# Kernel optimization log

Hardware: AMD Instinct MI355X
Metric: run time of the kernel (lower is better)

## Reference

```python
import jax, jax.numpy as jnp
import numpy as np

B, N, H = 2, 8192, 128
EPS = 1e-06


def setup_inputs() -> dict:
    key = jax.random.key(0)
    k1, k2, k3, k4 = jax.random.split(key, 4)
    x = jax.random.normal(k1, (B, N, H), dtype=jnp.float32)
    # adjacency is sparse in the original (tf.sparse); represented dense here
    # for the reference math (same result as sparse_dense_matmul).
    adj = jax.random.normal(k2, (B, N, N), dtype=jnp.float32)
    W = jax.random.normal(k3, (H, H), dtype=jnp.float32)
    b = jax.random.normal(k4, (H,), dtype=jnp.float32)
    return {"x": x, "adj": adj, "W": W, "b": b}


def reference(x, adj, W, b):
    # in-degree over |adj|, per batch, per node: [B, N]
    in_degrees = jnp.sum(jnp.abs(adj), axis=-1)
    # symmetric-ish degree normalization: [B, N, 1]
    norm = jnp.power(in_degrees + EPS, -0.5)[..., None]
    # dense projection: [B, N, H]
    support = jnp.matmul(x, W)
    # batched SpMM (dense equivalent) with pre/post degree norm
    out = jnp.einsum("bmn,bnh->bmh", adj, support * norm) * norm
    return jax.nn.elu(out + b)
```

## Files before the change

### kernel.cpp

```cpp
#include <hip/hip_runtime.h>
#include <hip/hip_bf16.h>
#include <math.h>

#define NN 8192
#define HD 128
#define NB 2
#define EPSF 1e-6f
#define BM 32
#define BK 128
#define NSTEP (NN / BK)

typedef __attribute__((ext_vector_type(8))) __bf16 bf16x8;
typedef __attribute__((ext_vector_type(4))) float f32x4;

__global__ __launch_bounds__(256) void k_degree(const float* __restrict__ adj,
                                                float* __restrict__ norm) {
    const int row  = blockIdx.x * 4 + (threadIdx.x >> 6);
    const int lane = threadIdx.x & 63;
    const float4* p = (const float4*)(adj + (size_t)row * NN);
    float s = 0.f;
#pragma unroll
    for (int i = 0; i < 32; ++i) {
        float4 v = p[(size_t)i * 64 + lane];
        s += fabsf(v.x) + fabsf(v.y) + fabsf(v.z) + fabsf(v.w);
    }
#pragma unroll
    for (int off = 32; off > 0; off >>= 1) s += __shfl_down(s, off);
    if (lane == 0) norm[row] = rsqrtf(s + EPSF);
}

__global__ __launch_bounds__(256) void k_support(const float* __restrict__ x,
                                                 const float* __restrict__ W,
                                                 const float* __restrict__ norm,
                                                 __hip_bfloat16* __restrict__ snT) {
    const int b  = blockIdx.x >> 9;
    const int n0 = (blockIdx.x & 511) * 16;
    __shared__ float xs[16][132];
    const int t = threadIdx.x;
    {
        const int r = t >> 4, c0 = (t & 15) * 8;
        const float* src = x + ((size_t)(b * NN + n0 + r)) * HD + c0;
        *(float4*)&xs[r][c0]     = *(const float4*)src;
        *(float4*)&xs[r][c0 + 4] = *(const float4*)(src + 4);
    }
    __syncthreads();
    const int nl = t & 15;
    const int h0 = (t >> 4) * 8;
    float s[8] = {0.f,0.f,0.f,0.f,0.f,0.f,0.f,0.f};
#pragma unroll 4
    for (int k = 0; k < HD; ++k) {
        const float xv = xs[nl][k];
        const float* wr = W + k * HD + h0;
        float4 wa = *(const float4*)wr;
        float4 wb = *(const float4*)(wr + 4);
        s[0] += xv * wa.x; s[1] += xv * wa.y; s[2] += xv * wa.z; s[3] += xv * wa.w;
        s[4] += xv * wb.x; s[5] += xv * wb.y; s[6] += xv * wb.z; s[7] += xv * wb.w;
    }
    const float nv = norm[b * NN + n0 + nl];
#pragma unroll
    for (int hb = 0; hb < 8; ++hb)
        snT[((size_t)b * HD + h0 + hb) * NN + n0 + nl] = __float2bfloat16(s[hb] * nv);
}

__device__ __forceinline__ bf16x8 cvt8(float4 a, float4 b) {
    bf16x8 r;
    r[0] = (__bf16)a.x; r[1] = (__bf16)a.y; r[2] = (__bf16)a.z; r[3] = (__bf16)a.w;
    r[4] = (__bf16)b.x; r[5] = (__bf16)b.y; r[6] = (__bf16)b.z; r[7] = (__bf16)b.w;
    return r;
}

__device__ __forceinline__ void gload_lds16(const float* g, void* l) {
    __builtin_amdgcn_global_load_lds(
        (const __attribute__((address_space(1))) void*)g,
        (__attribute__((address_space(3))) void*)l, 16, 0, 0);
}

__global__ __launch_bounds__(256, 4) void k_gemm8(const float* __restrict__ adj,
                                                  const __hip_bfloat16* __restrict__ snT,
                                                  const float* __restrict__ norm,
                                                  const float* __restrict__ bias,
                                                  float* __restrict__ out) {
    const int b    = blockIdx.y;
    const int swz  = (blockIdx.x & 7) * 32 + (blockIdx.x >> 3);
    const int m0   = swz * BM;
    const int w    = threadIdx.x >> 6;
    const int lane = threadIdx.x & 63;
    const int fr   = lane & 15;
    const int g    = lane >> 4;

    const float* adjB = adj + (size_t)b * NN * NN;
    const __hip_bfloat16* snB = snT + (size_t)b * HD * NN;

    __shared__ __align__(16) char Abuf[2][BM * BK * 4];

    const float* sptr[4];
#pragma unroll
    for (int c = 0; c < 4; ++c) {
        const int fg   = (w * 4 + c) * 64 + lane;
        const int row  = fg >> 5;
        const int gsrc = (fg & 31) ^ (row & 7);
        sptr[c] = adjB + (size_t)(m0 + row) * NN + gsrc * 4;
    }

    const __hip_bfloat16* bp0 = snB + (size_t)(w * 32 + fr) * NN + g * 8;
    const __hip_bfloat16* bp1 = bp0 + (size_t)16 * NN;

    f32x4 acc[2][2] = {};
    const int xr = fr & 7;

#pragma unroll
    for (int c = 0; c < 4; ++c)
        gload_lds16(sptr[c], &Abuf[0][(w * 4 + c) * 1024]);

#pragma unroll 1
    for (int s = 0; s < NSTEP; ++s) {
        __syncthreads();
        const char* lb = Abuf[s & 1];

        bf16x8 Bf[2][4];
#pragma unroll
        for (int ks = 0; ks < 4; ++ks) {
            Bf[0][ks] = *(const bf16x8*)(bp0 + s * BK + ks * 32);
            Bf[1][ks] = *(const bf16x8*)(bp1 + s * BK + ks * 32);
        }

        if (s + 1 < NSTEP) {
            char* nb = Abuf[(s + 1) & 1];
#pragma unroll
            for (int c = 0; c < 4; ++c)
                gload_lds16(sptr[c] + (s + 1) * BK, &nb[(w * 4 + c) * 1024]);
        }

#pragma unroll
        for (int mt = 0; mt < 2; ++mt) {
            const char* rbase = lb + (mt * 16 + fr) * 512;
#pragma unroll
            for (int ks = 0; ks < 4; ++ks) {
                float4 fa = *(const float4*)(rbase + ((ks * 8 + ((g * 2 + 0) ^ xr)) << 4));
                float4 fb = *(const float4*)(rbase + ((ks * 8 + ((g * 2 + 1) ^ xr)) << 4));
                bf16x8 af = cvt8(fa, fb);
                acc[mt][0] = __builtin_amdgcn_mfma_f32_16x16x32_bf16(af, Bf[0][ks], acc[mt][0], 0, 0, 0);
                acc[mt][1] = __builtin_amdgcn_mfma_f32_16x16x32_bf16(af, Bf[1][ks], acc[mt][1], 0, 0, 0);
            }
        }
    }

    const float* normB = norm + b * NN + m0;
    float* outB = out + ((size_t)b * NN + m0) * HD;
#pragma unroll
    for (int mt = 0; mt < 2; ++mt)
#pragma unroll
        for (int ht = 0; ht < 2; ++ht) {
            const int h  = w * 32 + ht * 16 + fr;
            const float bv = bias[h];
#pragma unroll
            for (int j = 0; j < 4; ++j) {
                const int r = mt * 16 + g * 4 + j;
                float v = acc[mt][ht][j] * normB[r] + bv;
                v = v > 0.f ? v : expm1f(v);
                outB[(size_t)r * HD + h] = v;
            }
        }
}

extern "C" void kernel_launch(void* const* d_in, const int* in_sizes, int n_in,
                              void* d_out, int out_size, void* d_ws, size_t ws_size,
                              hipStream_t stream) {
    (void)in_sizes; (void)n_in; (void)out_size; (void)ws_size;
    const float* x    = (const float*)d_in[0];
    const float* adj  = (const float*)d_in[1];
    const float* W    = (const float*)d_in[2];
    const float* bias = (const float*)d_in[3];
    float* out = (float*)d_out;

    float* norm = (float*)d_ws;
    __hip_bfloat16* snT = (__hip_bfloat16*)((char*)d_ws + 65536);

    k_degree <<<dim3(NB * NN / 4),  dim3(256), 0, stream>>>(adj, norm);
    k_support<<<dim3(NB * NN / 16), dim3(256), 0, stream>>>(x, W, norm, snT);
    k_gemm8  <<<dim3(NN / BM, NB),  dim3(256), 0, stream>>>(adj, snT, norm, bias, out);
}
```

Before: 280.2 us.

## Deepen adjacency prefetch to four LDS stages with register double-buffered B fragments

```diff
diff --git a/kernel.cpp b/kernel.cpp
--- a/kernel.cpp
+++ b/kernel.cpp
@@ -75,7 +75,7 @@
         (__attribute__((address_space(3))) void*)l, 16, 0, 0);
 }
 
-__global__ __launch_bounds__(256, 4) void k_gemm8(const float* __restrict__ adj,
+__global__ __launch_bounds__(256, 2) void k_gemm9(const float* __restrict__ adj,
                                                   const __hip_bfloat16* __restrict__ snT,
                                                   const float* __restrict__ norm,
                                                   const float* __restrict__ bias,
@@ -91,7 +91,7 @@
     const float* adjB = adj + (size_t)b * NN * NN;
     const __hip_bfloat16* snB = snT + (size_t)b * HD * NN;
 
-    __shared__ __align__(16) char Abuf[2][BM * BK * 4];
+    __shared__ __align__(16) char Abuf[4][BM * BK * 4];
 
     const float* sptr[4];
 #pragma unroll
@@ -107,43 +107,69 @@
 
     f32x4 acc[2][2] = {};
     const int xr = fr & 7;
-
-#pragma unroll
-    for (int c = 0; c < 4; ++c)
-        gload_lds16(sptr[c], &Abuf[0][(w * 4 + c) * 1024]);
+    bf16x8 BfA[2][4], BfB[2][4];
+
+#define STAGE(idx) do {                                                       \
+        char* nb_ = Abuf[(idx) & 3];                                          \
+        _Pragma("unroll")                                                     \
+        for (int c = 0; c < 4; ++c)                                           \
+            gload_lds16(sptr[c] + (idx) * BK, &nb_[(w * 4 + c) * 1024]);      \
+    } while (0)
+#define LOADB(BX, idx) do {                                                   \
+        _Pragma("unroll")                                                     \
+        for (int ks = 0; ks < 4; ++ks) {                                      \
+            BX[0][ks] = *(const bf16x8*)(bp0 + (idx) * BK + ks * 32);         \
+            BX[1][ks] = *(const bf16x8*)(bp1 + (idx) * BK + ks * 32);         \
+        }                                                                     \
+    } while (0)
+#define WAITN(n) asm volatile("s_waitcnt vmcnt(" #n ")" ::: "memory")
+#define BAR() do { __builtin_amdgcn_s_barrier();                              \
+                   __builtin_amdgcn_sched_barrier(0); } while (0)
+#define COMPUTE(kidx, BX) do {                                                \
+        const char* lb_ = Abuf[(kidx) & 3];                                   \
+        _Pragma("unroll")                                                     \
+        for (int mt = 0; mt < 2; ++mt) {                                      \
+            const char* rbase_ = lb_ + (mt * 16 + fr) * 512;                  \
+            _Pragma("unroll")                                                 \
+            for (int ks = 0; ks < 4; ++ks) {                                  \
+                float4 fa_ = *(const float4*)(rbase_ + ((ks * 8 + ((g * 2 + 0) ^ xr)) << 4)); \
+                float4 fb_ = *(const float4*)(rbase_ + ((ks * 8 + ((g * 2 + 1) ^ xr)) << 4)); \
+                bf16x8 af_ = cvt8(fa_, fb_);                                  \
+                acc[mt][0] = __builtin_amdgcn_mfma_f32_16x16x32_bf16(af_, BX[0][ks], acc[mt][0], 0, 0, 0); \
+                acc[mt][1] = __builtin_amdgcn_mfma_f32_16x16x32_bf16(af_, BX[1][ks], acc[mt][1], 0, 0, 0); \
+            }                                                                 \
+        }                                                                     \
+    } while (0)
+
+    STAGE(0);
+    STAGE(1);
+    LOADB(BfA, 0);
 
 #pragma unroll 1
-    for (int s = 0; s < NSTEP; ++s) {
-        __syncthreads();
-        const char* lb = Abuf[s & 1];
-
-        bf16x8 Bf[2][4];
-#pragma unroll
-        for (int ks = 0; ks < 4; ++ks) {
-            Bf[0][ks] = *(const bf16x8*)(bp0 + s * BK + ks * 32);
-            Bf[1][ks] = *(const bf16x8*)(bp1 + s * BK + ks * 32);
-        }
-
-        if (s + 1 < NSTEP) {
-            char* nb = Abuf[(s + 1) & 1];
-#pragma unroll
-            for (int c = 0; c < 4; ++c)
-                gload_lds16(sptr[c] + (s + 1) * BK, &nb[(w * 4 + c) * 1024]);
-        }
-
-#pragma unroll
-        for (int mt = 0; mt < 2; ++mt) {
-            const char* rbase = lb + (mt * 16 + fr) * 512;
-#pragma unroll
-            for (int ks = 0; ks < 4; ++ks) {
-                float4 fa = *(const float4*)(rbase + ((ks * 8 + ((g * 2 + 0) ^ xr)) << 4));
-                float4 fb = *(const float4*)(rbase + ((ks * 8 + ((g * 2 + 1) ^ xr)) << 4));
-                bf16x8 af = cvt8(fa, fb);
-                acc[mt][0] = __builtin_amdgcn_mfma_f32_16x16x32_bf16(af, Bf[0][ks], acc[mt][0], 0, 0, 0);
-                acc[mt][1] = __builtin_amdgcn_mfma_f32_16x16x32_bf16(af, Bf[1][ks], acc[mt][1], 0, 0, 0);
-            }
-        }
-    }
+    for (int k = 0; k < NSTEP - 3; k += 2) {
+        LOADB(BfB, k + 1);
+        STAGE(k + 2);
+        WAITN(16); BAR();
+        COMPUTE(k, BfA);
+
+        LOADB(BfA, k + 2);
+        STAGE(k + 3);
+        WAITN(16); BAR();
+        COMPUTE(k + 1, BfB);
+    }
+
+    LOADB(BfB, NSTEP - 1);
+    WAITN(0); BAR();
+    COMPUTE(NSTEP - 2, BfA);
+
+    WAITN(0); BAR();
+    COMPUTE(NSTEP - 1, BfB);
+
+#undef STAGE
+#undef LOADB
+#undef WAITN
+#undef BAR
+#undef COMPUTE
 
     const float* normB = norm + b * NN + m0;
     float* outB = out + ((size_t)b * NN + m0) * HD;
@@ -178,5 +204,5 @@
 
     k_degree <<<dim3(NB * NN / 4),  dim3(256), 0, stream>>>(adj, norm);
     k_support<<<dim3(NB * NN / 16), dim3(256), 0, stream>>>(x, W, norm, snT);
-    k_gemm8  <<<dim3(NN / BM, NB),  dim3(256), 0, stream>>>(adj, snT, norm, bias, out);
-}
+    k_gemm9  <<<dim3(NN / BM, NB),  dim3(256), 0, stream>>>(adj, snT, norm, bias, out);
+}
```

Result: faster. 274.6 us (-2.0%).
